# Optimization experiments

Measured on AMD Instinct MI355X. Metric: run time of the kernel, lower is better.

The kernel has to match this reference:

```python
import jax, jax.numpy as jnp
import numpy as np

DIM = 1024
D_INNER = 1024
D_STATE = 2048


def setup_inputs() -> dict:
    key = jax.random.key(0)
    ks = jax.random.split(key, 6)
    Bsz, T = 8, 2048
    x = jax.random.normal(ks[0], (Bsz, T, DIM), dtype=jnp.float32)
    h0 = jnp.zeros((Bsz, D_STATE), dtype=jnp.float32)
    # parameters (mamba2_init: normal std=0.02, log_A = 0)
    W_in = jax.random.normal(ks[1], (2 * D_INNER, DIM), dtype=jnp.float32) * 0.02   # nn.Linear weight [out,in]
    W_out = jax.random.normal(ks[2], (DIM, D_INNER), dtype=jnp.float32) * 0.02
    B_mat = jax.random.normal(ks[3], (D_INNER, D_STATE), dtype=jnp.float32) * 0.02
    C_mat = jax.random.normal(ks[4], (D_STATE, D_INNER), dtype=jnp.float32) * 0.02
    log_A = jnp.zeros((D_STATE,), dtype=jnp.float32)
    return {"x": x, "h0": h0, "W_in": W_in, "W_out": W_out,
            "B_mat": B_mat, "C_mat": C_mat, "log_A": log_A}


def reference(x, h0, W_in, W_out, B_mat, C_mat, log_A):
    # x: [B, T, dim]
    xz = jnp.einsum('btd,ed->bte', x, W_in)          # [B, T, 2*d_inner]
    x_proj, z = jnp.split(xz, 2, axis=-1)
    x_proj = jax.nn.silu(x_proj)
    A = jax.nn.sigmoid(log_A)                         # [d_state], fixed (non-selective)

    x_t = jnp.swapaxes(x_proj, 0, 1)                  # [T, B, d_inner]
    z_t = jnp.swapaxes(z, 0, 1)                       # [T, B, d_inner]

    def step(h, xz_t):
        xt, zt = xz_t
        h_new = jnp.tanh(A * h + xt @ B_mat)          # [B, d_state]
        y = (h_new @ C_mat) * jax.nn.silu(zt)         # [B, d_inner]
        return h_new, y

    h_final, y_seq = jax.lax.scan(step, h0, (x_t, z_t))  # y_seq: [T, B, d_inner]
    y = jnp.swapaxes(y_seq, 0, 1)                     # [B, T, d_inner]
    output = jnp.einsum('bti,oi->bto', y, W_out)      # [B, T, dim]
    return output, h_final
```

## Files before the change

kernel.cpp:

```cpp
#include <hip/hip_runtime.h>
#include <cstdint>
#include <cstddef>

#define DIM    1024
#define DINNER 1024
#define DSTATE 2048
#define BSZ    8
#define TLEN   2048
#define MROWS  (BSZ * TLEN)

typedef unsigned short u16;
typedef __attribute__((ext_vector_type(8))) __bf16 bf16x8;
typedef __attribute__((ext_vector_type(4))) float  f32x4;
typedef __attribute__((ext_vector_type(8))) u16    u16x8;

static __device__ __forceinline__ u16 f2bf(float f) {
  union { float f; uint32_t u; } v; v.f = f;
  uint32_t u = v.u;
  return (u16)((u + 0x7fffu + ((u >> 16) & 1u)) >> 16);
}

static __device__ __forceinline__ float bf2f(u16 b) {
  union { uint32_t u; float f; } v; v.u = ((uint32_t)b) << 16;
  return v.f;
}

static __device__ __forceinline__ float silu(float x) {
  return x / (1.f + __expf(-x));
}

__global__ void sentinel(float* out) { out[0] = 12345.0f; }


__global__ void cast_bf16x8(const float* __restrict__ in, u16* __restrict__ out, long n) {
  long i = ((long)blockIdx.x * blockDim.x + threadIdx.x) * 8;
  if (i >= n) return;
  float4 a = *(const float4*)(in + i);
  float4 b = *(const float4*)(in + i + 4);
  u16x8 o;
  o[0] = f2bf(a.x); o[1] = f2bf(a.y); o[2] = f2bf(a.z); o[3] = f2bf(a.w);
  o[4] = f2bf(b.x); o[5] = f2bf(b.y); o[6] = f2bf(b.z); o[7] = f2bf(b.w);
  *(u16x8*)(out + i) = o;
}

__global__ void transpose_cast(const float* __restrict__ in, u16* __restrict__ out,
                               int R, int C) {
  __shared__ float t[32][33];
  int c0 = blockIdx.x * 32, r0 = blockIdx.y * 32;
  int tx = threadIdx.x, ty = threadIdx.y;
#pragma unroll
  for (int i = 0; i < 32; i += 8)
    t[ty + i][tx] = in[(size_t)(r0 + ty + i) * C + c0 + tx];
  __syncthreads();
#pragma unroll
  for (int i = 0; i < 32; i += 8)
    out[(size_t)(c0 + ty + i) * R + r0 + tx] = f2bf(t[tx][ty + i]);
}


#define SEG  128
#define WARM 32

__global__ void __launch_bounds__(256) winscan(const u16* __restrict__ xB,
                                               u16* __restrict__ H,
                                               const float* __restrict__ h0,
                                               const float* __restrict__ logA,
                                               float* __restrict__ hf,
                                               int b0) {
  const int NSEG = TLEN / SEG;
  int tid  = blockIdx.x * 256 + threadIdx.x;
  int s    = tid & (DSTATE - 1);
  int rest = tid >> 11;
  int bl   = rest >> 4;
  int seg  = rest & (NSEG - 1);

  const float C2  = 2.8853900817779268f;
  const float L2E = 1.4426950408889634f;
  float A  = __builtin_amdgcn_rcpf(1.f + __builtin_amdgcn_exp2f(-logA[s] * L2E));
  float Ac = A * C2;

  const int t0 = seg * SEG;
  float h;
  const u16* src;
  if (seg == 0) {
    h = h0[(size_t)(b0 + bl) * DSTATE + s];
    src = xB + ((size_t)bl * TLEN) * DSTATE + s;
  } else {
    h = 0.f;
    src = xB + ((size_t)bl * TLEN + (t0 - WARM)) * DSTATE + s;
#pragma unroll
    for (int i = 0; i < WARM; ++i) {
      float g = fmaf(Ac, h, bf2f(src[(size_t)i * DSTATE]) * C2);
      float e = __builtin_amdgcn_exp2f(g);
      float r = __builtin_amdgcn_rcpf(e + 1.f);
      h = fmaf(-2.f, r, 1.f);
    }
    src += (size_t)WARM * DSTATE;
  }

  u16* dst = H + ((size_t)bl * TLEN + t0) * DSTATE + s;
  const int PF = 8;
  float buf[PF], nbuf[PF];
#pragma unroll
  for (int i = 0; i < PF; ++i) buf[i] = bf2f(src[(size_t)i * DSTATE]) * C2;
  for (int tc = 0; tc < SEG; tc += PF) {
    if (tc + PF < SEG) {
#pragma unroll
      for (int i = 0; i < PF; ++i) nbuf[i] = bf2f(src[(size_t)(tc + PF + i) * DSTATE]) * C2;
    }
#pragma unroll
    for (int i = 0; i < PF; ++i) {
      float g = fmaf(Ac, h, buf[i]);
      float e = __builtin_amdgcn_exp2f(g);
      float r = __builtin_amdgcn_rcpf(e + 1.f);
      h = fmaf(-2.f, r, 1.f);
      dst[(size_t)(tc + i) * DSTATE] = f2bf(h);
    }
#pragma unroll
    for (int i = 0; i < PF; ++i) buf[i] = nbuf[i];
  }
  if (seg == NSEG - 1) hf[(size_t)(b0 + bl) * DSTATE + s] = h;
}


enum { EPI_F32 = 0, EPI_SILU_SPLIT = 1, EPI_BF16 = 2, EPI_MUL_SZ = 3 };

#define GBAR()  __builtin_amdgcn_s_barrier()
#define LGKM0() do { asm volatile("s_waitcnt lgkmcnt(0)" ::: "memory"); \
                     __builtin_amdgcn_sched_barrier(0); } while (0)

template <int EPI>
__global__ void __launch_bounds__(512, 2) gemm256(const u16* __restrict__ A,
                                                  const u16* __restrict__ B,
                                                  float* __restrict__ Cf,
                                                  u16* __restrict__ O1,
                                                  u16* __restrict__ O2,
                                                  const u16* __restrict__ SZ,
                                                  int M, int N, int K) {
  extern __shared__ u16 lds[];
  const int tid = threadIdx.x, wid = tid >> 6, lane = tid & 63;
  const int wm = wid >> 2, wn = wid & 3;

  int bx = blockIdx.x, by = blockIdx.y;
  {
    int gx = gridDim.x, gy = gridDim.y;
    int nwg = gx * gy;
    int wg  = blockIdx.y * gx + blockIdx.x;
    if ((nwg & 7) == 0) {
      int v = (wg & 7) * (nwg >> 3) + (wg >> 3);
      bx = v / gy;
      by = v - bx * gy;
    }
  }
  const int m0 = bx * 256, n0 = by * 256;

  const int fr = lane & 15;
  const int kbs8 = ((lane >> 4) ^ ((fr >> 1) & 3)) * 8;
  const int srow = tid >> 2, skb = tid & 3;

  f32x4 acc[8][4] = {};
  bf16x8 af[8], bfj[4];

  auto STG = [&](int db, int mat, int ks, int kt) {
#pragma unroll
    for (int c = 0; c < 2; ++c) {
      int row = c * 128 + srow;
      int ksrc8 = (skb ^ ((row >> 1) & 3)) * 8;
      const u16* P = mat ? B : A;
      const u16* g = P + (size_t)((mat ? n0 : m0) + row) * K + (kt << 6) + (ks << 5) + ksrc8;
      u16* d = lds + (((db * 2 + mat) * 2 + ks) << 13) + (c << 12) + (wid << 9);
      __builtin_amdgcn_global_load_lds((const __attribute__((address_space(1))) void*)g,
          (__attribute__((address_space(3))) void*)d, 16, 0, 0);
    }
  };
  auto LDA = [&](int db, int ks) {
    const u16* base = lds + (((db * 2 + 0) * 2 + ks) << 13) + (wm * 128 + fr) * 32 + kbs8;
#pragma unroll
    for (int i = 0; i < 8; ++i) af[i] = *(const bf16x8*)(base + i * 512);
  };
  auto LDB2 = [&](int db, int ks, int jp) {
    const u16* base = lds + (((db * 2 + 1) * 2 + ks) << 13) + (wn * 64 + jp * 32 + fr) * 32 + kbs8;
#pragma unroll
    for (int j = 0; j < 2; ++j) bfj[jp * 2 + j] = *(const bf16x8*)(base + j * 512);
  };
  auto MM = [&](int jp) {
    __builtin_amdgcn_s_setprio(1);
#pragma unroll
    for (int i = 0; i < 8; ++i) {
      acc[i][jp * 2]     = __builtin_amdgcn_mfma_f32_16x16x32_bf16(af[i], bfj[jp * 2],     acc[i][jp * 2],     0, 0, 0);
      acc[i][jp * 2 + 1] = __builtin_amdgcn_mfma_f32_16x16x32_bf16(af[i], bfj[jp * 2 + 1], acc[i][jp * 2 + 1], 0, 0, 0);
    }
    __builtin_amdgcn_s_setprio(0);
  };

  const int T = K >> 6;
  const int I = T >> 1;

  STG(0, 0, 0, 0); STG(0, 1, 0, 0); STG(0, 0, 1, 0); STG(0, 1, 1, 0);
  STG(1, 0, 0, 1); STG(1, 1, 0, 1); STG(1, 0, 1, 1);
  asm volatile("s_waitcnt vmcnt(6)" ::: "memory");
  GBAR();

  for (int it = 0; it < I; ++it) {
    const bool last = (it == I - 1);
    const int t1 = 2 * it + 1, t2 = 2 * it + 2, t3 = 2 * it + 3;

    LDA(0, 0); LDB2(0, 0, 0); STG(1, 1, 1, t1);
    GBAR(); LGKM0(); MM(0); GBAR();
    LDB2(0, 0, 1); if (!last) STG(0, 0, 0, t2);
    GBAR(); LGKM0(); MM(1); GBAR();
    LDA(0, 1); LDB2(0, 1, 0); if (!last) STG(0, 1, 0, t2);
    GBAR(); LGKM0(); MM(0); GBAR();
    LDB2(0, 1, 1); if (!last) STG(0, 0, 1, t2);
    if (last) { asm volatile("s_waitcnt vmcnt(0)" ::: "memory"); }
    else      { asm volatile("s_waitcnt vmcnt(6)" ::: "memory"); }
    GBAR(); LGKM0(); MM(1); GBAR();
    LDA(1, 0); LDB2(1, 0, 0); if (!last) STG(0, 1, 1, t2);
    GBAR(); LGKM0(); MM(0); GBAR();
    LDB2(1, 0, 1); if (!last) STG(1, 0, 0, t3);
    GBAR(); LGKM0(); MM(1); GBAR();
    LDA(1, 1); LDB2(1, 1, 0); if (!last) STG(1, 1, 0, t3);
    GBAR(); LGKM0(); MM(0); GBAR();
    LDB2(1, 1, 1); if (!last) { STG(1, 0, 1, t3); asm volatile("s_waitcnt vmcnt(6)" ::: "memory"); }
    GBAR(); LGKM0(); MM(1); GBAR();
  }

  {
    float* esl = (float*)lds + wid * (16 * 66);
    const int cr = (lane >> 4) * 4;
    const int cc = lane & 15;
    const int erow = lane >> 2;
    const int ecol = (lane & 3) * 16;
#pragma unroll
    for (int i = 0; i < 8; ++i) {
#pragma unroll
      for (int j = 0; j < 4; ++j)
#pragma unroll
        for (int r = 0; r < 4; ++r)
          esl[(cr + r) * 66 + j * 16 + cc] = acc[i][j][r];
      asm volatile("s_waitcnt lgkmcnt(0)" ::: "memory");
      __builtin_amdgcn_sched_barrier(0);
      f32x4 v0 = *(const f32x4*)(esl + erow * 66 + ecol);
      f32x4 v1 = *(const f32x4*)(esl + erow * 66 + ecol + 4);
      f32x4 v2 = *(const f32x4*)(esl + erow * 66 + ecol + 8);
      f32x4 v3 = *(const f32x4*)(esl + erow * 66 + ecol + 12);
      asm volatile("s_waitcnt lgkmcnt(0)" ::: "memory");
      __builtin_amdgcn_sched_barrier(0);
      const int gm = m0 + wm * 128 + i * 16 + erow;
      const int gn = n0 + wn * 64 + ecol;
      if constexpr (EPI == EPI_F32) {
        float* cp = Cf + (size_t)gm * N + gn;
        *(f32x4*)(cp)      = v0;
        *(f32x4*)(cp + 4)  = v1;
        *(f32x4*)(cp + 8)  = v2;
        *(f32x4*)(cp + 12) = v3;
      } else if constexpr (EPI == EPI_BF16) {
        u16x8 o1, o2;
#pragma unroll
        for (int r = 0; r < 4; ++r) { o1[r] = f2bf(v0[r]); o1[4 + r] = f2bf(v1[r]); }
#pragma unroll
        for (int r = 0; r < 4; ++r) { o2[r] = f2bf(v2[r]); o2[4 + r] = f2bf(v3[r]); }
        u16* op = O1 + (size_t)gm * N + gn;
        *(u16x8*)(op) = o1;
        *(u16x8*)(op + 8) = o2;
      } else if constexpr (EPI == EPI_SILU_SPLIT) {
        u16x8 o1, o2;
#pragma unroll
        for (int r = 0; r < 4; ++r) { o1[r] = f2bf(silu(v0[r])); o1[4 + r] = f2bf(silu(v1[r])); }
#pragma unroll
        for (int r = 0; r < 4; ++r) { o2[r] = f2bf(silu(v2[r])); o2[4 + r] = f2bf(silu(v3[r])); }
        const int half = N >> 1;
        u16* op = (gn < half ? O1 + (size_t)gm * half + gn
                             : O2 + (size_t)gm * half + (gn - half));
        *(u16x8*)(op) = o1;
        *(u16x8*)(op + 8) = o2;
      } else {
        const u16* sp = SZ + (size_t)gm * N + gn;
        u16x8 s1 = *(const u16x8*)(sp);
        u16x8 s2 = *(const u16x8*)(sp + 8);
        u16x8 o1, o2;
#pragma unroll
        for (int r = 0; r < 4; ++r) { o1[r] = f2bf(v0[r] * bf2f(s1[r])); o1[4 + r] = f2bf(v1[r] * bf2f(s1[4 + r])); }
#pragma unroll
        for (int r = 0; r < 4; ++r) { o2[r] = f2bf(v2[r] * bf2f(s2[r])); o2[4 + r] = f2bf(v3[r] * bf2f(s2[4 + r])); }
        u16* op = O1 + (size_t)gm * N + gn;
        *(u16x8*)(op) = o1;
        *(u16x8*)(op + 8) = o2;
      }
    }
  }
}


extern "C" void kernel_launch(void* const* d_in, const int* in_sizes, int n_in,
                              void* d_out, int out_size, void* d_ws, size_t ws_size,
                              hipStream_t stream) {
  const float* x     = (const float*)d_in[0];
  const float* h0    = (const float*)d_in[1];
  const float* W_in  = (const float*)d_in[2];
  const float* W_out = (const float*)d_in[3];
  const float* Bm    = (const float*)d_in[4];
  const float* Cm    = (const float*)d_in[5];
  const float* logA  = (const float*)d_in[6];
  float* out = (float*)d_out;
  float* hf  = out + (size_t)MROWS * DIM;

  const int LDSB = 131072;
  hipFuncSetAttribute((const void*)gemm256<EPI_F32>,        hipFuncAttributeMaxDynamicSharedMemorySize, LDSB);
  hipFuncSetAttribute((const void*)gemm256<EPI_SILU_SPLIT>, hipFuncAttributeMaxDynamicSharedMemorySize, LDSB);
  hipFuncSetAttribute((const void*)gemm256<EPI_BF16>,       hipFuncAttributeMaxDynamicSharedMemorySize, LDSB);
  hipFuncSetAttribute((const void*)gemm256<EPI_MUL_SZ>,     hipFuncAttributeMaxDynamicSharedMemorySize, LDSB);

  auto align256 = [](size_t b) { return (b + 255) & ~(size_t)255; };

  const size_t w_win  = align256((size_t)2 * DINNER * DIM * 2);
  const size_t w_wout = align256((size_t)DIM * DINNER * 2);
  const size_t w_bt   = align256((size_t)DSTATE * DINNER * 2);
  const size_t w_ct   = align256((size_t)DINNER * DSTATE * 2);
  const size_t w_weights = w_win + w_wout + w_bt + w_ct;

  int nb = 0;
  const int cand[4] = {8, 4, 2, 1};
  size_t su = 0, sx = 0, ssz = 0, sxb = 0;
  for (int ci = 0; ci < 4; ++ci) {
    int c = cand[ci];
    size_t Mc = (size_t)c * TLEN;
    su  = (size_t)Mc * DINNER * 2;
    sx  = (size_t)Mc * DINNER * 2;
    ssz = (size_t)Mc * DINNER * 2;
    sxb = (size_t)Mc * DSTATE * 2;
    if (w_weights + su + sx + ssz + sxb <= ws_size) { nb = c; break; }
  }
  if (!nb) { sentinel<<<1, 1, 0, stream>>>(out); return; }

  char* ws = (char*)d_ws;
  u16* Win_bf  = (u16*)ws;             ws += w_win;
  u16* Wout_bf = (u16*)ws;             ws += w_wout;
  u16* BT_bf   = (u16*)ws;             ws += w_bt;
  u16* CT_bf   = (u16*)ws;             ws += w_ct;
  u16* u_bf    = (u16*)ws;             ws += su;
  u16* x_bf    = (u16*)ws;             ws += sx;
  u16* sz_bf   = (u16*)ws;             ws += ssz;
  u16* xB_bf   = (u16*)ws;             ws += sxb;
  u16* H_bf    = u_bf;
  u16* y_bf    = xB_bf;

  cast_bf16x8<<<(2 * DINNER * DIM) / 8 / 256, 256, 0, stream>>>(W_in, Win_bf, (long)2 * DINNER * DIM);
  cast_bf16x8<<<(DIM * DINNER) / 8 / 256, 256, 0, stream>>>(W_out, Wout_bf, (long)DIM * DINNER);
  transpose_cast<<<dim3(DSTATE / 32, DINNER / 32), dim3(32, 8), 0, stream>>>(Bm, BT_bf, DINNER, DSTATE);
  transpose_cast<<<dim3(DINNER / 32, DSTATE / 32), dim3(32, 8), 0, stream>>>(Cm, CT_bf, DSTATE, DINNER);

  for (int b0 = 0; b0 < BSZ; b0 += nb) {
    const int Mc = nb * TLEN;
    const float* xc = x + (size_t)b0 * TLEN * DIM;
    float* outc = out + (size_t)b0 * TLEN * DIM;

    cast_bf16x8<<<((size_t)Mc * DIM) / 8 / 256, 256, 0, stream>>>(xc, x_bf, (long)Mc * DIM);

    gemm256<EPI_SILU_SPLIT><<<dim3(Mc / 256, (2 * DINNER) / 256), 512, LDSB, stream>>>(
        x_bf, Win_bf, nullptr, u_bf, sz_bf, nullptr, Mc, 2 * DINNER, DIM);

    gemm256<EPI_BF16><<<dim3(Mc / 256, DSTATE / 256), 512, LDSB, stream>>>(
        u_bf, BT_bf, nullptr, xB_bf, nullptr, nullptr, Mc, DSTATE, DINNER);

    winscan<<<Mc / 16, 256, 0, stream>>>(xB_bf, H_bf, h0, logA, hf, b0);

    gemm256<EPI_MUL_SZ><<<dim3(Mc / 256, DINNER / 256), 512, LDSB, stream>>>(
        H_bf, CT_bf, nullptr, y_bf, nullptr, sz_bf, Mc, DINNER, DSTATE);

    gemm256<EPI_F32><<<dim3(Mc / 256, DIM / 256), 512, LDSB, stream>>>(
        y_bf, Wout_bf, outc, nullptr, nullptr, nullptr, Mc, DIM, DINNER);
  }
}
```

Baseline: 342.9 us.

## Load all B fragments at once and cut barriers in GEMM main loop

Replaces the two-half B fragment loads with a single four-fragment load per k-substep, so each LDS read phase is followed by two MFMA groups with no load in between. Barriers drop from two per MFMA group to one, and async global-to-LDS stages are reissued right after the barrier. The goal is less synchronization stall and better overlap of MFMA with memory traffic. The cost is higher register pressure from holding more B fragments, and correctness now depends on a subtler barrier placement around LDS buffer reuse.

```diff
diff --git a/kernel.cpp b/kernel.cpp
--- a/kernel.cpp
+++ b/kernel.cpp
@@ -178,10 +178,10 @@
 #pragma unroll
     for (int i = 0; i < 8; ++i) af[i] = *(const bf16x8*)(base + i * 512);
   };
-  auto LDB2 = [&](int db, int ks, int jp) {
-    const u16* base = lds + (((db * 2 + 1) * 2 + ks) << 13) + (wn * 64 + jp * 32 + fr) * 32 + kbs8;
-#pragma unroll
-    for (int j = 0; j < 2; ++j) bfj[jp * 2 + j] = *(const bf16x8*)(base + j * 512);
+  auto LDB4 = [&](int db, int ks) {
+    const u16* base = lds + (((db * 2 + 1) * 2 + ks) << 13) + (wn * 64 + fr) * 32 + kbs8;
+#pragma unroll
+    for (int j = 0; j < 4; ++j) bfj[j] = *(const bf16x8*)(base + j * 512);
   };
   auto MM = [&](int jp) {
     __builtin_amdgcn_s_setprio(1);
@@ -199,31 +199,33 @@
   STG(0, 0, 0, 0); STG(0, 1, 0, 0); STG(0, 0, 1, 0); STG(0, 1, 1, 0);
   STG(1, 0, 0, 1); STG(1, 1, 0, 1); STG(1, 0, 1, 1);
   asm volatile("s_waitcnt vmcnt(6)" ::: "memory");
-  GBAR();
 
   for (int it = 0; it < I; ++it) {
     const bool last = (it == I - 1);
     const int t1 = 2 * it + 1, t2 = 2 * it + 2, t3 = 2 * it + 3;
 
-    LDA(0, 0); LDB2(0, 0, 0); STG(1, 1, 1, t1);
-    GBAR(); LGKM0(); MM(0); GBAR();
-    LDB2(0, 0, 1); if (!last) STG(0, 0, 0, t2);
-    GBAR(); LGKM0(); MM(1); GBAR();
-    LDA(0, 1); LDB2(0, 1, 0); if (!last) STG(0, 1, 0, t2);
-    GBAR(); LGKM0(); MM(0); GBAR();
-    LDB2(0, 1, 1); if (!last) STG(0, 0, 1, t2);
+    GBAR(); STG(1, 1, 1, t1); LDA(0, 0); LDB4(0, 0);
+    LGKM0(); MM(0);
+    GBAR(); if (!last) STG(0, 0, 0, t2); MM(1);
+
+    GBAR(); if (!last) STG(0, 1, 0, t2); LDA(0, 1); LDB4(0, 1);
+    LGKM0(); MM(0);
+    GBAR(); if (!last) STG(0, 0, 1, t2);
     if (last) { asm volatile("s_waitcnt vmcnt(0)" ::: "memory"); }
     else      { asm volatile("s_waitcnt vmcnt(6)" ::: "memory"); }
-    GBAR(); LGKM0(); MM(1); GBAR();
-    LDA(1, 0); LDB2(1, 0, 0); if (!last) STG(0, 1, 1, t2);
-    GBAR(); LGKM0(); MM(0); GBAR();
-    LDB2(1, 0, 1); if (!last) STG(1, 0, 0, t3);
-    GBAR(); LGKM0(); MM(1); GBAR();
-    LDA(1, 1); LDB2(1, 1, 0); if (!last) STG(1, 1, 0, t3);
-    GBAR(); LGKM0(); MM(0); GBAR();
-    LDB2(1, 1, 1); if (!last) { STG(1, 0, 1, t3); asm volatile("s_waitcnt vmcnt(6)" ::: "memory"); }
-    GBAR(); LGKM0(); MM(1); GBAR();
-  }
+    MM(1);
+
+    GBAR(); if (!last) STG(0, 1, 1, t2); LDA(1, 0); LDB4(1, 0);
+    LGKM0(); MM(0);
+    GBAR(); if (!last) STG(1, 0, 0, t3); MM(1);
+
+    GBAR(); if (!last) STG(1, 1, 0, t3); LDA(1, 1); LDB4(1, 1);
+    LGKM0(); MM(0);
+    GBAR();
+    if (!last) { STG(1, 0, 1, t3); asm volatile("s_waitcnt vmcnt(6)" ::: "memory"); }
+    MM(1);
+  }
+  GBAR();
 
   {
     float* esl = (float*)lds + wid * (16 * 66);
```

After: 339.1 us. No clear change (-1.1%).
